# Performance work log

Measured on AMD Instinct MI355X. Metric: run time of the kernel, lower is better.

## Reference

```python
import jax, jax.numpy as jnp
import numpy as np

ITERATIONS = 4


def setup_inputs() -> dict:
    key = jax.random.key(0)
    x = jax.random.normal(key, (256, 512, 256), dtype=jnp.float32)
    return {"x": x}


def reference(x):
    # axis == 1 branch of the torch module (default)
    N, len_m, len_d = x.shape
    m = jnp.mean(x, axis=1, keepdims=True)          # [N, 1, D]
    xn = x - m                                      # [N, M, D]
    # sigma = xn^T xn / (M - 1)  -> [N, D, D]
    sigma = jnp.einsum('nmd,nme->nde', xn, xn) / (len_m - 1)

    # trace-normalized Newton-Schulz iteration for inverse sqrt
    trace = jnp.trace(sigma, axis1=-2, axis2=-1)[:, None, None]  # [N, 1, 1]
    sigma_norm = sigma / trace
    P = jnp.broadcast_to(jnp.eye(len_d, dtype=x.dtype), (N, len_d, len_d))
    for _ in range(ITERATIONS):
        P3 = P @ P @ P                              # matrix_power(P, 3), batched
        P = 1.5 * P - 0.5 * (P3 @ sigma_norm)
    wm = P / jnp.sqrt(trace)                        # whitening matrix [N, D, D]

    decorrelated = xn @ wm                          # [N, M, D]
    return decorrelated
```

## Files before the change

kernel.cpp:

```cpp
#include <hip/hip_runtime.h>
#include <stdint.h>

#define Nn 256
#define Mm 512
#define Dd 256

typedef unsigned short u16;
typedef unsigned int u32;
typedef __attribute__((ext_vector_type(8))) short bf16x8;
typedef __attribute__((ext_vector_type(4))) float f32x4;

#define AGPR_W(dst, src) asm volatile("v_accvgpr_write_b32 %0, %1" : "=a"(dst) : "v"(src))
#define AGPR_R(dst, src) asm volatile("v_accvgpr_read_b32 %0, %1" : "=v"(dst) : "a"(src))

__device__ __forceinline__ u16 f2b(float f) {
    unsigned u = __float_as_uint(f);
    return (u16)((u + 0x7FFFu + ((u >> 16) & 1u)) >> 16);
}
__device__ __forceinline__ float b2f(u16 h) {
    return __uint_as_float(((unsigned)h) << 16);
}
__device__ __forceinline__ u32 pk2(float lo, float hi) {
    return (u32)f2b(lo) | ((u32)f2b(hi) << 16);
}
__device__ __forceinline__ void glds16(const u16* g, u16* l) {
    __builtin_amdgcn_global_load_lds((const __attribute__((address_space(1))) void*)g,
                                     (__attribute__((address_space(3))) void*)l, 16, 0, 0);
}

__global__ __launch_bounds__(256) void mean_part_kernel(const float* __restrict__ x,
                                                        float* __restrict__ meanPart) {
    const int bid = blockIdx.x;
    const int n = bid >> 2, c = bid & 3;
    const int tid = threadIdx.x;
    const float* xb = x + (size_t)n * Mm * Dd + (size_t)c * 128 * Dd;
    float a0 = 0.f, a1 = 0.f, a2 = 0.f, a3 = 0.f;
    for (int m = 0; m < 128; m += 4) {
        a0 += xb[(m + 0) * Dd + tid];
        a1 += xb[(m + 1) * Dd + tid];
        a2 += xb[(m + 2) * Dd + tid];
        a3 += xb[(m + 3) * Dd + tid];
    }
    meanPart[((size_t)n * 4 + c) * Dd + tid] = a0 + a1 + a2 + a3;
}

__global__ __launch_bounds__(256) void center_tr_kernel(const float* __restrict__ x,
                                                        const float* __restrict__ meanPart,
                                                        u16* __restrict__ xn,
                                                        u16* __restrict__ xnT) {
    __shared__ float meanS[Dd];
    __shared__ u16 tileS[64 * 66];
    const int bid = blockIdx.x;
    const int n = bid >> 3, mt = bid & 7;
    const int tid = threadIdx.x;

    const float* mp = meanPart + (size_t)n * 4 * Dd;
    meanS[tid] = (mp[tid] + mp[Dd + tid] + mp[2 * Dd + tid] + mp[3 * Dd + tid]) * (1.0f / Mm);
    __syncthreads();

    const float* xb = x + (size_t)n * Mm * Dd;
    u16* xnb = xn + (size_t)n * Mm * Dd;
    u16* xtb = xnT + (size_t)n * Dd * Mm;
    const int mrow = tid >> 4, dq = tid & 15;
    const int tx2 = (tid & 31) * 2, ty = tid >> 5;

    for (int dt = 0; dt < Dd / 64; ++dt) {
        #pragma unroll
        for (int rr = 0; rr < 4; ++rr) {
            int ml = mrow + 16 * rr;
            int m = mt * 64 + ml;
            int d = dt * 64 + dq * 4;
            float4 v = *(const float4*)(xb + (size_t)m * Dd + d);
            float4 mu = *(const float4*)(meanS + d);
            u16 b0 = f2b(v.x - mu.x), b1 = f2b(v.y - mu.y);
            u16 b2 = f2b(v.z - mu.z), b3 = f2b(v.w - mu.w);
            u32 lo = (u32)b0 | ((u32)b1 << 16);
            u32 hi = (u32)b2 | ((u32)b3 << 16);
            *(uint2*)(xnb + (size_t)m * Dd + d) = make_uint2(lo, hi);
            tileS[(dq * 4 + 0) * 66 + ml] = b0;
            tileS[(dq * 4 + 1) * 66 + ml] = b1;
            tileS[(dq * 4 + 2) * 66 + ml] = b2;
            tileS[(dq * 4 + 3) * 66 + ml] = b3;
        }
        __syncthreads();
        #pragma unroll
        for (int r = 0; r < 8; ++r) {
            int dl = r * 8 + ty;
            u32 w = *(const u32*)(tileS + dl * 66 + tx2);
            *(u32*)(xtb + (size_t)(dt * 64 + dl) * Mm + mt * 64 + tx2) = w;
        }
        __syncthreads();
    }
}

__global__ __launch_bounds__(256) void sigma_kernel(const u16* __restrict__ xnT,
                                                    float* __restrict__ sigma) {
    __shared__ u16 sA[128 * 32];
    __shared__ u16 sB[128 * 32];
    const int bid = blockIdx.x;
    const int xcd = bid & 7, slot = bid >> 3;
    const int t = slot & 3;
    const int n = ((slot >> 2) << 3) | xcd;
    const int tr = t >> 1, tc = t & 1;
    const int tid = threadIdx.x;
    const int lane = tid & 63, wave = tid >> 6;
    const int wr = wave >> 1, wc = wave & 1;
    const int l15 = lane & 15, quad = lane >> 4;
    const int row0 = tid >> 2, q = tid & 3;
    const int wb8 = (tid & 192) * 8;

    const u16* base = xnT + (size_t)n * Dd * Mm;
    const u16* gA = base + (size_t)(tr * 128) * Mm;
    const u16* gB = base + (size_t)(tc * 128) * Mm;

    f32x4 acc[4][4];
    #pragma unroll
    for (int i = 0; i < 4; ++i)
        #pragma unroll
        for (int j = 0; j < 4; ++j) acc[i][j] = (f32x4){0.f, 0.f, 0.f, 0.f};

    for (int kk = 0; kk < Mm; kk += 32) {
        glds16(gA + (size_t)row0 * Mm + kk + q * 8, sA + wb8);
        glds16(gA + (size_t)(row0 + 64) * Mm + kk + q * 8, sA + 2048 + wb8);
        glds16(gB + (size_t)row0 * Mm + kk + q * 8, sB + wb8);
        glds16(gB + (size_t)(row0 + 64) * Mm + kk + q * 8, sB + 2048 + wb8);
        __syncthreads();
        bf16x8 a[4], b[4];
        #pragma unroll
        for (int i = 0; i < 4; ++i) a[i] = *(const bf16x8*)(sA + (wr * 64 + i * 16 + l15) * 32 + quad * 8);
        #pragma unroll
        for (int j = 0; j < 4; ++j) b[j] = *(const bf16x8*)(sB + (wc * 64 + j * 16 + l15) * 32 + quad * 8);
        #pragma unroll
        for (int i = 0; i < 4; ++i)
            #pragma unroll
            for (int j = 0; j < 4; ++j)
                acc[i][j] = __builtin_amdgcn_mfma_f32_16x16x32_bf16(a[i], b[j], acc[i][j], 0, 0, 0);
        __syncthreads();
    }

    float* sg = sigma + (size_t)n * Dd * Dd;
    #pragma unroll
    for (int i = 0; i < 4; ++i)
        #pragma unroll
        for (int j = 0; j < 4; ++j)
            #pragma unroll
            for (int r = 0; r < 4; ++r) {
                int row = tr * 128 + wr * 64 + i * 16 + quad * 4 + r;
                int col = tc * 128 + wc * 64 + j * 16 + l15;
                sg[row * Dd + col] = acc[i][j][r];
            }
}

__device__ __forceinline__ bf16x8 ldP(const u16* Plds, int row, int ch) {
    return *(const bf16x8*)(Plds + row * 256 + ((ch ^ (row & 7)) << 3));
}

__global__ __launch_bounds__(1024, 4) void ns_chain_kernel(const float* __restrict__ sigma,
                                                           u16* __restrict__ Wg,
                                                           u16* __restrict__ Sh,
                                                           u16* __restrict__ Sl) {
    __shared__ __align__(16) u16 lds[81920];
    u16* Plds = lds;
    u16* strips = lds + 65536;
    u16* sQ = strips;
    u16* sA = strips;
    u16* sS = strips + 8192;

    const int n = blockIdx.x, tid = threadIdx.x;
    const int lane = tid & 63, wave = tid >> 6;
    const int l15 = lane & 15, quad = lane >> 4;
    const int wr8 = wave >> 1, wc2 = wave & 1;

    const float* sg = sigma + (size_t)n * 65536;
    u16* shp = Sh + (size_t)n * 65536;
    u16* slp = Sl + (size_t)n * 65536;

    float* red = (float*)strips;
    if (tid < 256) red[tid] = sg[tid * 257];
    __syncthreads();
    for (int s = 128; s > 0; s >>= 1) {
        if (tid < s) red[tid] += red[tid + s];
        __syncthreads();
    }
    const float inv = 1.0f / red[0];
    const float rtr = sqrtf(511.0f * inv);

    #pragma unroll 4
    for (int itp = 0; itp < 16; ++itp) {
        int idx = itp * 4096 + tid * 4;
        float4 v = *(const float4*)(sg + idx);
        int row = idx >> 8, col = idx & 255;
        float s0 = v.x * inv, s1 = v.y * inv, s2 = v.z * inv, s3 = v.w * inv;
        u16 h0 = f2b(s0), h1 = f2b(s1), h2 = f2b(s2), h3 = f2b(s3);
        *(uint2*)(shp + idx) = make_uint2((u32)h0 | ((u32)h1 << 16), (u32)h2 | ((u32)h3 << 16));
        u16 e0 = f2b(s0 - b2f(h0)), e1 = f2b(s1 - b2f(h1));
        u16 e2 = f2b(s2 - b2f(h2)), e3 = f2b(s3 - b2f(h3));
        *(uint2*)(slp + idx) = make_uint2((u32)e0 | ((u32)e1 << 16), (u32)e2 | ((u32)e3 << 16));
        u16 p0 = f2b(((row == col + 0) ? 1.5f : 0.f) - 0.5f * s0);
        u16 p1 = f2b(((row == col + 1) ? 1.5f : 0.f) - 0.5f * s1);
        u16 p2 = f2b(((row == col + 2) ? 1.5f : 0.f) - 0.5f * s2);
        u16 p3 = f2b(((row == col + 3) ? 1.5f : 0.f) - 0.5f * s3);
        int pa = row * 256 + (((col >> 3) ^ (row & 7)) << 3) + (col & 7);
        *(uint2*)(Plds + pa) = make_uint2((u32)p0 | ((u32)p1 << 16), (u32)p2 | ((u32)p3 << 16));
    }
    __syncthreads();

    const u16* sBase = (wave < 8) ? shp : slp;
    const int w8 = wave & 7;
    const int cl_st = w8 * 16 + (lane >> 2);
    const int gch_st = (lane & 3) ^ (cl_st & 3);
    u16* sDst = sS + ((wave < 8) ? 0 : 4096) + w8 * 512 + lane * 8;

    #pragma unroll 1
    for (int it = 0; it < 3; ++it) {
        const bool last = (it == 2);
        u32 p3a[32];

        #pragma unroll
        for (int jp = 0; jp < 4; ++jp) {
            {
                f32x4 acc1[4];
                #pragma unroll
                for (int jj = 0; jj < 4; ++jj) acc1[jj] = (f32x4){0.f, 0.f, 0.f, 0.f};
                #pragma unroll
                for (int s = 0; s < 8; ++s) {
                    bf16x8 a = ldP(Plds, wave * 16 + l15, s * 4 + quad);
                    #pragma unroll
                    for (int jj = 0; jj < 4; ++jj) {
                        bf16x8 b = ldP(Plds, jp * 64 + jj * 16 + l15, s * 4 + quad);
                        acc1[jj] = __builtin_amdgcn_mfma_f32_16x16x32_bf16(a, b, acc1[jj], 0, 0, 0);
                    }
                }
                #pragma unroll
                for (int jj = 0; jj < 4; ++jj) {
                    int cl = jj * 16 + l15;
                    int k0 = wave * 16 + quad * 4;
                    int addr = cl * 256 + (((k0 >> 3) ^ (cl & 7)) << 3) + (k0 & 7);
                    *(uint2*)(sQ + addr) = make_uint2(pk2(acc1[jj][0], acc1[jj][1]),
                                                      pk2(acc1[jj][2], acc1[jj][3]));
                }
            }
            __syncthreads();
            {
                f32x4 acc2[4];
                #pragma unroll
                for (int jj = 0; jj < 4; ++jj) acc2[jj] = (f32x4){0.f, 0.f, 0.f, 0.f};
                #pragma unroll
                for (int s = 0; s < 8; ++s) {
                    bf16x8 a = ldP(Plds, wave * 16 + l15, s * 4 + quad);
                    #pragma unroll
                    for (int jj = 0; jj < 4; ++jj) {
                        int cl = jj * 16 + l15;
                        bf16x8 b = *(const bf16x8*)(sQ + cl * 256 + (((s * 4 + quad) ^ (cl & 7)) << 3));
                        acc2[jj] = __builtin_amdgcn_mfma_f32_16x16x32_bf16(a, b, acc2[jj], 0, 0, 0);
                    }
                }
                #pragma unroll
                for (int jj = 0; jj < 4; ++jj)
                    #pragma unroll
                    for (int rh = 0; rh < 2; ++rh)
                        AGPR_W(p3a[(jp * 4 + jj) * 2 + rh], pk2(acc2[jj][2 * rh], acc2[jj][2 * rh + 1]));
            }
            __syncthreads();
        }

        uint4 gregA = *(const uint4*)(sBase + (size_t)cl_st * 256 + gch_st * 8);
        uint4 gregB = *(const uint4*)(sBase + (size_t)cl_st * 256 + 32 + gch_st * 8);
        #pragma unroll 1
        for (int jc = 0; jc < 2; ++jc) {
            f32x4 acc3[2][4];
            #pragma unroll
            for (int i16 = 0; i16 < 2; ++i16)
                #pragma unroll
                for (int j = 0; j < 4; ++j) acc3[i16][j] = (f32x4){0.f, 0.f, 0.f, 0.f};
            #pragma unroll
            for (int s = 0; s < 8; ++s) {
                #pragma unroll
                for (int jjh = 0; jjh < 2; ++jjh) {
                    int jjsrc = (s & 1) * 2 + jjh;
                    int kloc = jjh * 16 + l15;
                    int ch = kloc >> 3, k7 = kloc & 7;
                    #pragma unroll
                    for (int rh = 0; rh < 2; ++rh) {
                        u32 wv;
                        AGPR_R(wv, p3a[((s >> 1) * 4 + jjsrc) * 2 + rh]);
                        #pragma unroll
                        for (int bit = 0; bit < 2; ++bit) {
                            int row = wave * 16 + quad * 4 + 2 * rh + bit;
                            int sw = (row ^ (row >> 2)) & 3;
                            sA[row * 32 + ((ch ^ sw) << 3) + k7] =
                                (u16)(bit ? (wv >> 16) : (wv & 0xffffu));
                        }
                    }
                }
                if ((s & 1) == 0) {
                    *(uint4*)sDst = gregA;
                    int t2 = jc * 8 + s + 2;
                    if (t2 < 16) {
                        int jcn = t2 >> 3, sn = t2 & 7;
                        gregA = *(const uint4*)(sBase + (size_t)(jcn * 128 + cl_st) * 256 + sn * 32 + gch_st * 8);
                    }
                } else {
                    *(uint4*)sDst = gregB;
                    int t2 = jc * 8 + s + 2;
                    if (t2 < 16) {
                        int jcn = t2 >> 3, sn = t2 & 7;
                        gregB = *(const uint4*)(sBase + (size_t)(jcn * 128 + cl_st) * 256 + sn * 32 + gch_st * 8);
                    }
                }
                asm volatile("s_waitcnt lgkmcnt(0)" ::: "memory");
                __builtin_amdgcn_s_barrier();
                {
                    bf16x8 a[2];
                    #pragma unroll
                    for (int i16 = 0; i16 < 2; ++i16) {
                        int ar = wr8 * 32 + i16 * 16 + l15;
                        int asw = (ar ^ (ar >> 2)) & 3;
                        a[i16] = *(const bf16x8*)(sA + ar * 32 + ((quad ^ asw) << 3));
                    }
                    #pragma unroll
                    for (int j = 0; j < 4; ++j) {
                        int cl = wc2 * 64 + j * 16 + l15;
                        int co = cl * 32 + ((quad ^ (cl & 3)) << 3);
                        bf16x8 bh = *(const bf16x8*)(sS + co);
                        bf16x8 bl = *(const bf16x8*)(sS + 4096 + co);
                        #pragma unroll
                        for (int i16 = 0; i16 < 2; ++i16)
                            acc3[i16][j] = __builtin_amdgcn_mfma_f32_16x16x32_bf16(a[i16], bh, acc3[i16][j], 0, 0, 0);
                        #pragma unroll
                        for (int i16 = 0; i16 < 2; ++i16)
                            acc3[i16][j] = __builtin_amdgcn_mfma_f32_16x16x32_bf16(a[i16], bl, acc3[i16][j], 0, 0, 0);
                    }
                }
                asm volatile("s_waitcnt lgkmcnt(0)" ::: "memory");
                __builtin_amdgcn_s_barrier();
            }
            #pragma unroll
            for (int i16 = 0; i16 < 2; ++i16)
                #pragma unroll
                for (int j = 0; j < 4; ++j)
                    #pragma unroll
                    for (int r = 0; r < 4; ++r) {
                        int row = wr8 * 32 + i16 * 16 + quad * 4 + r;
                        int col = jc * 128 + wc2 * 64 + j * 16 + l15;
                        int pa = row * 256 + (((col >> 3) ^ (row & 7)) << 3) + (col & 7);
                        float pv = 1.5f * b2f(Plds[pa]) - 0.5f * acc3[i16][j][r];
                        Plds[pa] = f2b(last ? pv * rtr : pv);
                    }
        }
        __syncthreads();
    }

    u16* wg = Wg + (size_t)n * 65536;
    #pragma unroll
    for (int q = 0; q < 8; ++q) {
        int f = q * 1024 + tid;
        int row = f >> 5, ch = f & 31;
        uint4 v = *(const uint4*)(Plds + row * 256 + ((ch ^ (row & 7)) << 3));
        *(uint4*)(wg + row * 256 + ch * 8) = v;
    }
}

__global__ __launch_bounds__(256) void final_gemm(const u16* __restrict__ xn,
                                                  const u16* __restrict__ Wh,
                                                  float* __restrict__ out) {
    __shared__ u16 sA[128 * 32];
    __shared__ u16 sB[128 * 32];
    const int bid = blockIdx.x;
    const int xcd = bid & 7, slot = bid >> 3;
    const int t = slot & 7;
    const int n = ((slot >> 3) << 3) | xcd;
    const int tr = t >> 1, tc = t & 1;
    const int tid = threadIdx.x;
    const int lane = tid & 63, wave = tid >> 6;
    const int wr = wave >> 1, wc = wave & 1;
    const int l15 = lane & 15, quad = lane >> 4;
    const int row0 = tid >> 2, q = tid & 3;
    const int wb8 = (tid & 192) * 8;

    const u16* gA = xn + (size_t)n * Mm * Dd + (size_t)(tr * 128) * Dd;
    const u16* gB = Wh + (size_t)n * Dd * Dd + (size_t)(tc * 128) * Dd;

    f32x4 acc[4][4];
    #pragma unroll
    for (int i = 0; i < 4; ++i)
        #pragma unroll
        for (int j = 0; j < 4; ++j) acc[i][j] = (f32x4){0.f, 0.f, 0.f, 0.f};

    for (int kk = 0; kk < Dd; kk += 32) {
        glds16(gA + (size_t)row0 * Dd + kk + q * 8, sA + wb8);
        glds16(gA + (size_t)(row0 + 64) * Dd + kk + q * 8, sA + 2048 + wb8);
        glds16(gB + (size_t)row0 * Dd + kk + q * 8, sB + wb8);
        glds16(gB + (size_t)(row0 + 64) * Dd + kk + q * 8, sB + 2048 + wb8);
        __syncthreads();
        bf16x8 a[4], b[4];
        #pragma unroll
        for (int i = 0; i < 4; ++i) a[i] = *(const bf16x8*)(sA + (wr * 64 + i * 16 + l15) * 32 + quad * 8);
        #pragma unroll
        for (int j = 0; j < 4; ++j) b[j] = *(const bf16x8*)(sB + (wc * 64 + j * 16 + l15) * 32 + quad * 8);
        #pragma unroll
        for (int i = 0; i < 4; ++i)
            #pragma unroll
            for (int j = 0; j < 4; ++j)
                acc[i][j] = __builtin_amdgcn_mfma_f32_16x16x32_bf16(a[i], b[j], acc[i][j], 0, 0, 0);
        __syncthreads();
    }

    float* ob = out + (size_t)n * Mm * Dd;
    #pragma unroll
    for (int i = 0; i < 4; ++i)
        #pragma unroll
        for (int j = 0; j < 4; ++j)
            #pragma unroll
            for (int r = 0; r < 4; ++r) {
                int row = tr * 128 + wr * 64 + i * 16 + quad * 4 + r;
                int col = tc * 128 + wc * 64 + j * 16 + l15;
                ob[(size_t)row * Dd + col] = acc[i][j][r];
            }
}

extern "C" void kernel_launch(void* const* d_in, const int* in_sizes, int n_in,
                              void* d_out, int out_size, void* d_ws, size_t ws_size,
                              hipStream_t stream) {
    const float* x = (const float*)d_in[0];
    float* out = (float*)d_out;
    char* ws = (char*)d_ws;
    const size_t MB32 = 33554432;

    u16* xn = (u16*)(ws + 0);
    u16* xnT = (u16*)(ws + 2 * MB32);
    u16* W = (u16*)(ws + 2 * MB32);
    float* sigma = (float*)(ws + 4 * MB32);
    u16* Sh = (u16*)(ws + 6 * MB32);
    u16* Sl = (u16*)(ws + 7 * MB32);
    float* meanPart = (float*)(ws + 9 * MB32);

    mean_part_kernel<<<Nn * 4, 256, 0, stream>>>(x, meanPart);
    center_tr_kernel<<<Nn * 8, 256, 0, stream>>>(x, meanPart, xn, xnT);
    sigma_kernel<<<Nn * 4, 256, 0, stream>>>(xnT, sigma);
    ns_chain_kernel<<<Nn, 1024, 0, stream>>>(sigma, W, Sh, Sl);
    final_gemm<<<Nn * 8, 256, 0, stream>>>(xn, W, out);
}
```

Before: 583.3 us.

## Halve NS-chain block to 512 threads with 32-row per-wave tiles

The Newton-Schulz chain kernel now runs with 8 waves instead of 16, and each wave owns a 32-row strip instead of 16 rows. The wave's A fragments of P are kept in registers across the jp loop. Each wave covers all 128 columns in the third GEMM, and the sigma strip staging loads two 16-byte chunks per lane. The P^3 staging is kept in a plain register array instead of explicit AGPR writes. The aim is more register reuse and fewer LDS reads per MFMA, at the cost of higher register pressure (64 packed words plus 16 fragments per thread) and half the threads to hide latency.

```diff
diff --git a/kernel.cpp b/kernel.cpp
--- a/kernel.cpp
+++ b/kernel.cpp
@@ -9,9 +9,6 @@
 typedef unsigned int u32;
 typedef __attribute__((ext_vector_type(8))) short bf16x8;
 typedef __attribute__((ext_vector_type(4))) float f32x4;
-
-#define AGPR_W(dst, src) asm volatile("v_accvgpr_write_b32 %0, %1" : "=a"(dst) : "v"(src))
-#define AGPR_R(dst, src) asm volatile("v_accvgpr_read_b32 %0, %1" : "=v"(dst) : "a"(src))
 
 __device__ __forceinline__ u16 f2b(float f) {
     unsigned u = __float_as_uint(f);
@@ -155,10 +152,10 @@
     return *(const bf16x8*)(Plds + row * 256 + ((ch ^ (row & 7)) << 3));
 }
 
-__global__ __launch_bounds__(1024, 4) void ns_chain_kernel(const float* __restrict__ sigma,
-                                                           u16* __restrict__ Wg,
-                                                           u16* __restrict__ Sh,
-                                                           u16* __restrict__ Sl) {
+__global__ __launch_bounds__(512, 2) void ns_chain_kernel(const float* __restrict__ sigma,
+                                                          u16* __restrict__ Wg,
+                                                          u16* __restrict__ Sh,
+                                                          u16* __restrict__ Sl) {
     __shared__ __align__(16) u16 lds[81920];
     u16* Plds = lds;
     u16* strips = lds + 65536;
@@ -169,7 +166,6 @@
     const int n = blockIdx.x, tid = threadIdx.x;
     const int lane = tid & 63, wave = tid >> 6;
     const int l15 = lane & 15, quad = lane >> 4;
-    const int wr8 = wave >> 1, wc2 = wave & 1;
 
     const float* sg = sigma + (size_t)n * 65536;
     u16* shp = Sh + (size_t)n * 65536;
@@ -186,8 +182,8 @@
     const float rtr = sqrtf(511.0f * inv);
 
     #pragma unroll 4
-    for (int itp = 0; itp < 16; ++itp) {
-        int idx = itp * 4096 + tid * 4;
+    for (int itp = 0; itp < 32; ++itp) {
+        int idx = itp * 2048 + tid * 4;
         float4 v = *(const float4*)(sg + idx);
         int row = idx >> 8, col = idx & 255;
         float s0 = v.x * inv, s1 = v.y * inv, s2 = v.z * inv, s3 = v.w * inv;
@@ -205,74 +201,101 @@
     }
     __syncthreads();
 
-    const u16* sBase = (wave < 8) ? shp : slp;
-    const int w8 = wave & 7;
-    const int cl_st = w8 * 16 + (lane >> 2);
-    const int gch_st = (lane & 3) ^ (cl_st & 3);
-    u16* sDst = sS + ((wave < 8) ? 0 : 4096) + w8 * 512 + lane * 8;
+    const u16* sBase = (wave < 4) ? shp : slp;
+    const int w4 = wave & 3;
+    const int cl_st = w4 * 32 + (lane >> 1);
+    const int c0 = (lane & 1) * 2;
+    const int kc0 = c0 ^ (cl_st & 3);
+    const int kc1 = (c0 + 1) ^ (cl_st & 3);
+    u16* sDst = sS + ((wave < 4) ? 0 : 4096) + cl_st * 32 + c0 * 8;
 
     #pragma unroll 1
     for (int it = 0; it < 3; ++it) {
         const bool last = (it == 2);
-        u32 p3a[32];
+        u32 p3a[64];
+
+        bf16x8 aF[2][8];
+        #pragma unroll
+        for (int i16 = 0; i16 < 2; ++i16)
+            #pragma unroll
+            for (int s = 0; s < 8; ++s)
+                aF[i16][s] = ldP(Plds, wave * 32 + i16 * 16 + l15, s * 4 + quad);
 
         #pragma unroll
         for (int jp = 0; jp < 4; ++jp) {
             {
-                f32x4 acc1[4];
-                #pragma unroll
-                for (int jj = 0; jj < 4; ++jj) acc1[jj] = (f32x4){0.f, 0.f, 0.f, 0.f};
+                f32x4 acc1[2][4];
+                #pragma unroll
+                for (int i16 = 0; i16 < 2; ++i16)
+                    #pragma unroll
+                    for (int jj = 0; jj < 4; ++jj) acc1[i16][jj] = (f32x4){0.f, 0.f, 0.f, 0.f};
                 #pragma unroll
                 for (int s = 0; s < 8; ++s) {
-                    bf16x8 a = ldP(Plds, wave * 16 + l15, s * 4 + quad);
+                    bf16x8 b[4];
+                    #pragma unroll
+                    for (int jj = 0; jj < 4; ++jj)
+                        b[jj] = ldP(Plds, jp * 64 + jj * 16 + l15, s * 4 + quad);
+                    #pragma unroll
+                    for (int i16 = 0; i16 < 2; ++i16)
+                        #pragma unroll
+                        for (int jj = 0; jj < 4; ++jj)
+                            acc1[i16][jj] = __builtin_amdgcn_mfma_f32_16x16x32_bf16(aF[i16][s], b[jj], acc1[i16][jj], 0, 0, 0);
+                }
+                #pragma unroll
+                for (int i16 = 0; i16 < 2; ++i16)
                     #pragma unroll
                     for (int jj = 0; jj < 4; ++jj) {
-                        bf16x8 b = ldP(Plds, jp * 64 + jj * 16 + l15, s * 4 + quad);
-                        acc1[jj] = __builtin_amdgcn_mfma_f32_16x16x32_bf16(a, b, acc1[jj], 0, 0, 0);
-                    }
-                }
-                #pragma unroll
-                for (int jj = 0; jj < 4; ++jj) {
-                    int cl = jj * 16 + l15;
-                    int k0 = wave * 16 + quad * 4;
-                    int addr = cl * 256 + (((k0 >> 3) ^ (cl & 7)) << 3) + (k0 & 7);
-                    *(uint2*)(sQ + addr) = make_uint2(pk2(acc1[jj][0], acc1[jj][1]),
-                                                      pk2(acc1[jj][2], acc1[jj][3]));
-                }
+                        int cl = jj * 16 + l15;
+                        int k0 = wave * 32 + i16 * 16 + quad * 4;
+                        int addr = cl * 256 + (((k0 >> 3) ^ (cl & 7)) << 3) + (k0 & 7);
+                        *(uint2*)(sQ + addr) = make_uint2(pk2(acc1[i16][jj][0], acc1[i16][jj][1]),
+                                                          pk2(acc1[i16][jj][2], acc1[i16][jj][3]));
+                    }
             }
             __syncthreads();
             {
-                f32x4 acc2[4];
-                #pragma unroll
-                for (int jj = 0; jj < 4; ++jj) acc2[jj] = (f32x4){0.f, 0.f, 0.f, 0.f};
+                f32x4 acc2[2][4];
+                #pragma unroll
+                for (int i16 = 0; i16 < 2; ++i16)
+                    #pragma unroll
+                    for (int jj = 0; jj < 4; ++jj) acc2[i16][jj] = (f32x4){0.f, 0.f, 0.f, 0.f};
                 #pragma unroll
                 for (int s = 0; s < 8; ++s) {
-                    bf16x8 a = ldP(Plds, wave * 16 + l15, s * 4 + quad);
+                    bf16x8 b[4];
                     #pragma unroll
                     for (int jj = 0; jj < 4; ++jj) {
                         int cl = jj * 16 + l15;
-                        bf16x8 b = *(const bf16x8*)(sQ + cl * 256 + (((s * 4 + quad) ^ (cl & 7)) << 3));
-                        acc2[jj] = __builtin_amdgcn_mfma_f32_16x16x32_bf16(a, b, acc2[jj], 0, 0, 0);
-                    }
+                        b[jj] = *(const bf16x8*)(sQ + cl * 256 + (((s * 4 + quad) ^ (cl & 7)) << 3));
+                    }
+                    #pragma unroll
+                    for (int i16 = 0; i16 < 2; ++i16)
+                        #pragma unroll
+                        for (int jj = 0; jj < 4; ++jj)
+                            acc2[i16][jj] = __builtin_amdgcn_mfma_f32_16x16x32_bf16(aF[i16][s], b[jj], acc2[i16][jj], 0, 0, 0);
                 }
                 #pragma unroll
-                for (int jj = 0; jj < 4; ++jj)
-                    #pragma unroll
-                    for (int rh = 0; rh < 2; ++rh)
-                        AGPR_W(p3a[(jp * 4 + jj) * 2 + rh], pk2(acc2[jj][2 * rh], acc2[jj][2 * rh + 1]));
+                for (int i16 = 0; i16 < 2; ++i16)
+                    #pragma unroll
+                    for (int jj = 0; jj < 4; ++jj)
+                        #pragma unroll
+                        for (int rh = 0; rh < 2; ++rh)
+                            p3a[((jp * 4 + jj) * 2 + i16) * 2 + rh] =
+                                pk2(acc2[i16][jj][2 * rh], acc2[i16][jj][2 * rh + 1]);
             }
             __syncthreads();
         }
 
-        uint4 gregA = *(const uint4*)(sBase + (size_t)cl_st * 256 + gch_st * 8);
-        uint4 gregB = *(const uint4*)(sBase + (size_t)cl_st * 256 + 32 + gch_st * 8);
+        uint4 gA0 = *(const uint4*)(sBase + (size_t)cl_st * 256 + kc0 * 8);
+        uint4 gA1 = *(const uint4*)(sBase + (size_t)cl_st * 256 + kc1 * 8);
+        uint4 gB0 = *(const uint4*)(sBase + (size_t)cl_st * 256 + 32 + kc0 * 8);
+        uint4 gB1 = *(const uint4*)(sBase + (size_t)cl_st * 256 + 32 + kc1 * 8);
         #pragma unroll 1
         for (int jc = 0; jc < 2; ++jc) {
-            f32x4 acc3[2][4];
+            f32x4 acc3[2][8];
             #pragma unroll
             for (int i16 = 0; i16 < 2; ++i16)
                 #pragma unroll
-                for (int j = 0; j < 4; ++j) acc3[i16][j] = (f32x4){0.f, 0.f, 0.f, 0.f};
+                for (int j = 0; j < 8; ++j) acc3[i16][j] = (f32x4){0.f, 0.f, 0.f, 0.f};
             #pragma unroll
             for (int s = 0; s < 8; ++s) {
                 #pragma unroll
@@ -281,31 +304,38 @@
                     int kloc = jjh * 16 + l15;
                     int ch = kloc >> 3, k7 = kloc & 7;
                     #pragma unroll
-                    for (int rh = 0; rh < 2; ++rh) {
-                        u32 wv;
-                        AGPR_R(wv, p3a[((s >> 1) * 4 + jjsrc) * 2 + rh]);
-                        #pragma unroll
-                        for (int bit = 0; bit < 2; ++bit) {
-                            int row = wave * 16 + quad * 4 + 2 * rh + bit;
-                            int sw = (row ^ (row >> 2)) & 3;
-                            sA[row * 32 + ((ch ^ sw) << 3) + k7] =
-                                (u16)(bit ? (wv >> 16) : (wv & 0xffffu));
+                    for (int i16 = 0; i16 < 2; ++i16)
+                        #pragma unroll
+                        for (int rh = 0; rh < 2; ++rh) {
+                            u32 wv = p3a[(((s >> 1) * 4 + jjsrc) * 2 + i16) * 2 + rh];
+                            #pragma unroll
+                            for (int bit = 0; bit < 2; ++bit) {
+                                int row = wave * 32 + i16 * 16 + quad * 4 + 2 * rh + bit;
+                                int sw = (row ^ (row >> 2)) & 3;
+                                sA[row * 32 + ((ch ^ sw) << 3) + k7] =
+                                    (u16)(bit ? (wv >> 16) : (wv & 0xffffu));
+                            }
                         }
-                    }
                 }
                 if ((s & 1) == 0) {
-                    *(uint4*)sDst = gregA;
+                    *(uint4*)sDst = gA0;
+                    *(uint4*)(sDst + 8) = gA1;
                     int t2 = jc * 8 + s + 2;
                     if (t2 < 16) {
                         int jcn = t2 >> 3, sn = t2 & 7;
-                        gregA = *(const uint4*)(sBase + (size_t)(jcn * 128 + cl_st) * 256 + sn * 32 + gch_st * 8);
+                        const u16* src = sBase + (size_t)(jcn * 128 + cl_st) * 256 + sn * 32;
+                        gA0 = *(const uint4*)(src + kc0 * 8);
+                        gA1 = *(const uint4*)(src + kc1 * 8);
                     }
                 } else {
-                    *(uint4*)sDst = gregB;
+                    *(uint4*)sDst = gB0;
+                    *(uint4*)(sDst + 8) = gB1;
                     int t2 = jc * 8 + s + 2;
                     if (t2 < 16) {
                         int jcn = t2 >> 3, sn = t2 & 7;
-                        gregB = *(const uint4*)(sBase + (size_t)(jcn * 128 + cl_st) * 256 + sn * 32 + gch_st * 8);
+                        const u16* src = sBase + (size_t)(jcn * 128 + cl_st) * 256 + sn * 32;
+                        gB0 = *(const uint4*)(src + kc0 * 8);
+                        gB1 = *(const uint4*)(src + kc1 * 8);
                     }
                 }
                 asm volatile("s_waitcnt lgkmcnt(0)" ::: "memory");
@@ -314,13 +344,13 @@
                     bf16x8 a[2];
                     #pragma unroll
                     for (int i16 = 0; i16 < 2; ++i16) {
-                        int ar = wr8 * 32 + i16 * 16 + l15;
+                        int ar = wave * 32 + i16 * 16 + l15;
                         int asw = (ar ^ (ar >> 2)) & 3;
                         a[i16] = *(const bf16x8*)(sA + ar * 32 + ((quad ^ asw) << 3));
                     }
                     #pragma unroll
-                    for (int j = 0; j < 4; ++j) {
-                        int cl = wc2 * 64 + j * 16 + l15;
+                    for (int j = 0; j < 8; ++j) {
+                        int cl = j * 16 + l15;
                         int co = cl * 32 + ((quad ^ (cl & 3)) << 3);
                         bf16x8 bh = *(const bf16x8*)(sS + co);
                         bf16x8 bl = *(const bf16x8*)(sS + 4096 + co);
@@ -338,11 +368,11 @@
             #pragma unroll
             for (int i16 = 0; i16 < 2; ++i16)
                 #pragma unroll
-                for (int j = 0; j < 4; ++j)
+                for (int j = 0; j < 8; ++j)
                     #pragma unroll
                     for (int r = 0; r < 4; ++r) {
-                        int row = wr8 * 32 + i16 * 16 + quad * 4 + r;
-                        int col = jc * 128 + wc2 * 64 + j * 16 + l15;
+                        int row = wave * 32 + i16 * 16 + quad * 4 + r;
+                        int col = jc * 128 + j * 16 + l15;
                         int pa = row * 256 + (((col >> 3) ^ (row & 7)) << 3) + (col & 7);
                         float pv = 1.5f * b2f(Plds[pa]) - 0.5f * acc3[i16][j][r];
                         Plds[pa] = f2b(last ? pv * rtr : pv);
@@ -353,8 +383,8 @@
 
     u16* wg = Wg + (size_t)n * 65536;
     #pragma unroll
-    for (int q = 0; q < 8; ++q) {
-        int f = q * 1024 + tid;
+    for (int q = 0; q < 16; ++q) {
+        int f = q * 512 + tid;
         int row = f >> 5, ch = f & 31;
         uint4 v = *(const uint4*)(Plds + row * 256 + ((ch ^ (row & 7)) << 3));
         *(uint4*)(wg + row * 256 + ch * 8) = v;
@@ -438,6 +468,6 @@
     mean_part_kernel<<<Nn * 4, 256, 0, stream>>>(x, meanPart);
     center_tr_kernel<<<Nn * 8, 256, 0, stream>>>(x, meanPart, xn, xnT);
     sigma_kernel<<<Nn * 4, 256, 0, stream>>>(xnT, sigma);
-    ns_chain_kernel<<<Nn, 1024, 0, stream>>>(sigma, W, Sh, Sl);
+    ns_chain_kernel<<<Nn, 512, 0, stream>>>(sigma, W, Sh, Sl);
     final_gemm<<<Nn * 8, 256, 0, stream>>>(xn, W, out);
 }
```

New measurement: 605.2 us. +3.8%, slower.
